# Performance work log

Measured on AMD Instinct MI355X. Metric: run time of the kernel, lower is better.

Reference implementation:

```python
import jax, jax.numpy as jnp
import numpy as np

MAX_GAP = 32  # n_index = 2*MAX_GAP+1 = 65


def setup_inputs() -> dict:
    key = jax.random.key(0)
    kW, kb = jax.random.split(key)
    B, S, E, N = 1, 1024, 128, 2 * MAX_GAP + 1
    idxs = jnp.arange(B * S, dtype=jnp.int64 if jax.config.jax_enable_x64 else jnp.int32).reshape(B, S)
    W = jax.random.normal(kW, (E, N), dtype=jnp.float32)  # nn.Linear weight (out, in)
    b = jax.random.normal(kb, (E,), dtype=jnp.float32)    # nn.Linear bias
    return {"idxs": idxs, "W": W, "b": b}


def reference(idxs, W, b):
    # pos_2d[b,i,j] = clip(idxs[b,j] - idxs[b,i], -max_gap, max_gap) + max_gap  in [0, n_index)
    pos = jnp.clip(idxs[:, None, :] - idxs[:, :, None], -MAX_GAP, MAX_GAP) + MAX_GAP  # (B,S,S)
    # onehot(pos) @ W.T + b  ==  row-gather from W.T plus bias (same math, no dense one-hot)
    return jnp.take(W.T, pos, axis=0) + b  # (B,S,S,E)
```

## Files before the change

### kernel.cpp

```cpp
#include <hip/hip_runtime.h>


#define MAXGAP 32
#define NIDX   65
#define EDIM   128
#define E4     32

__global__ __launch_bounds__(256) void relpos2d_kernel(
    const int* __restrict__ idxs,
    const float* __restrict__ W,
    const float* __restrict__ bias,
    float4* __restrict__ out,
    int S, int SS, int rows_total)
{
    __shared__ float table[NIDX][EDIM];

    for (int t = threadIdx.x; t < NIDX * EDIM; t += 256) {
        int p = t >> 7;
        int e = t & 127;
        table[p][e] = W[e * NIDX + p] + bias[e];
    }
    __syncthreads();

    const int lane4 = threadIdx.x & 31;
    const int rsub  = threadIdx.x >> 5;
    const int ROWS_PER_STEP = 256 / 32;

    for (int row = blockIdx.x * ROWS_PER_STEP + rsub; row < rows_total;
         row += gridDim.x * ROWS_PER_STEP) {
        int bi  = row / SS;
        int rem = row - bi * SS;
        int i   = rem / S;
        int j   = rem - i * S;

        int d = idxs[bi * S + j] - idxs[bi * S + i];
        d = d < -MAXGAP ? -MAXGAP : (d > MAXGAP ? MAXGAP : d);
        int p = d + MAXGAP;

        const float4* trow = reinterpret_cast<const float4*>(&table[p][0]);
        out[(size_t)row * E4 + lane4] = trow[lane4];
    }
}

extern "C" void kernel_launch(void* const* d_in, const int* in_sizes, int n_in,
                              void* d_out, int out_size, void* d_ws, size_t ws_size,
                              hipStream_t stream) {
    const int*   idxs = (const int*)  d_in[0];
    const float* W    = (const float*)d_in[1];
    const float* bias = (const float*)d_in[2];

    float* out = (float*)d_out;

    const int S  = in_sizes[0];
    const int SS = S * S;
    const int rows_total = SS;

    const int grid = 2048;
    relpos2d_kernel<<<grid, 256, 0, stream>>>(
        idxs, W, bias, (float4*)out, S, SS, rows_total);
}
```

Measured before the change: 112.3 us.

## Map blocks to row halves, cache idxs in LDS, use nontemporal stores

Reassigns each block to a fixed row i and half of the j range, removing per-element integer division and the repeated global idxs loads by staging the j indices in shared memory. Output writes use nontemporal stores to avoid polluting caches for the large streaming output. The grid size is now tied to S, and the extra shared array slightly raises LDS usage.

```diff
diff --git a/kernel.cpp b/kernel.cpp
--- a/kernel.cpp
+++ b/kernel.cpp
@@ -5,40 +5,50 @@
 #define NIDX   65
 #define EDIM   128
 #define E4     32
+#define CHUNKS 2
+
+typedef float f32x4 __attribute__((ext_vector_type(4)));
 
 __global__ __launch_bounds__(256) void relpos2d_kernel(
     const int* __restrict__ idxs,
     const float* __restrict__ W,
     const float* __restrict__ bias,
-    float4* __restrict__ out,
-    int S, int SS, int rows_total)
+    f32x4* __restrict__ out,
+    int S, int halfS)
 {
     __shared__ float table[NIDX][EDIM];
+    __shared__ int   jidx[1024];
 
     for (int t = threadIdx.x; t < NIDX * EDIM; t += 256) {
         int p = t >> 7;
         int e = t & 127;
         table[p][e] = W[e * NIDX + p] + bias[e];
     }
+
+    const int i     = blockIdx.x >> 1;
+    const int chunk = blockIdx.x & (CHUNKS - 1);
+    const int jbase = chunk * halfS;
+
+    for (int t = threadIdx.x; t < halfS; t += 256)
+        jidx[t] = idxs[jbase + t];
+
     __syncthreads();
 
     const int lane4 = threadIdx.x & 31;
-    const int rsub  = threadIdx.x >> 5;
-    const int ROWS_PER_STEP = 256 / 32;
+    const int jsub  = threadIdx.x >> 5;
+    const int idx_i = idxs[i];
 
-    for (int row = blockIdx.x * ROWS_PER_STEP + rsub; row < rows_total;
-         row += gridDim.x * ROWS_PER_STEP) {
-        int bi  = row / SS;
-        int rem = row - bi * SS;
-        int i   = rem / S;
-        int j   = rem - i * S;
+    f32x4* __restrict__ orow = out + (size_t)i * S * E4 + (size_t)jbase * E4;
 
-        int d = idxs[bi * S + j] - idxs[bi * S + i];
+    #pragma unroll 4
+    for (int jj = 0; jj < halfS; jj += 8) {
+        int j = jj + jsub;
+        int d = jidx[j] - idx_i;
         d = d < -MAXGAP ? -MAXGAP : (d > MAXGAP ? MAXGAP : d);
         int p = d + MAXGAP;
 
-        const float4* trow = reinterpret_cast<const float4*>(&table[p][0]);
-        out[(size_t)row * E4 + lane4] = trow[lane4];
+        f32x4 v = reinterpret_cast<const f32x4*>(&table[p][0])[lane4];
+        __builtin_nontemporal_store(v, &orow[(size_t)j * E4 + lane4]);
     }
 }
 
@@ -49,13 +59,11 @@
     const float* W    = (const float*)d_in[1];
     const float* bias = (const float*)d_in[2];
 
-    float* out = (float*)d_out;
+    f32x4* out = (f32x4*)d_out;
 
-    const int S  = in_sizes[0];
-    const int SS = S * S;
-    const int rows_total = SS;
+    const int S     = in_sizes[0];
+    const int halfS = S / 2;
+    const int grid  = S * CHUNKS;
 
-    const int grid = 2048;
-    relpos2d_kernel<<<grid, 256, 0, stream>>>(
-        idxs, W, bias, (float4*)out, S, SS, rows_total);
+    relpos2d_kernel<<<grid, 256, 0, stream>>>(idxs, W, bias, out, S, halfS);
 }
```

Result: faster. 103.6 us (-7.8%).
